# Optimization experiments

Hardware: AMD Instinct MI355X
Metric: run time of the kernel (lower is better)

## Reference

```python
import jax, jax.numpy as jnp
import numpy as np

EPS = 1e-5
NUM_GROUPS = 32


def setup_inputs() -> dict:
    key = jax.random.key(0)
    ks = jax.random.split(key, 4)
    b, c, h, w = 8, 512, 32, 32
    x = jax.random.normal(ks[0], (b, c, h, w), dtype=jnp.float32)
    gn_weight = jnp.ones((c,), dtype=jnp.float32)
    gn_bias = jnp.zeros((c,), dtype=jnp.float32)
    qkv_w = jax.random.normal(ks[1], (3 * c, c), dtype=jnp.float32) * (1.0 / np.sqrt(c))
    qkv_b = jnp.zeros((3 * c,), dtype=jnp.float32)
    proj_w = jax.random.normal(ks[2], (c, c), dtype=jnp.float32) * (1.0 / np.sqrt(c))
    proj_b = jnp.zeros((c,), dtype=jnp.float32)
    return {"x": x, "gn_weight": gn_weight, "gn_bias": gn_bias,
            "qkv_w": qkv_w, "qkv_b": qkv_b, "proj_w": proj_w, "proj_b": proj_b}


def _group_norm(x, weight, bias):
    b, c, h, w = x.shape
    xg = x.reshape(b, NUM_GROUPS, c // NUM_GROUPS, h, w)
    mean = xg.mean(axis=(2, 3, 4), keepdims=True)
    var = xg.var(axis=(2, 3, 4), keepdims=True)
    xn = ((xg - mean) * jax.lax.rsqrt(var + EPS)).reshape(b, c, h, w)
    return xn * weight[None, :, None, None] + bias[None, :, None, None]


def reference(x, gn_weight, gn_bias, qkv_w, qkv_b, proj_w, proj_b):
    b, c, h, w = x.shape
    scale = c ** (-0.5)
    xn = _group_norm(x, gn_weight, gn_bias)
    # 1x1 conv == per-pixel matmul over channels
    qkv = jnp.einsum('bchw,oc->bohw', xn, qkv_w) + qkv_b[None, :, None, None]
    q, k, v = jnp.split(qkv.reshape(b, 3 * c, h * w), 3, axis=1)  # each [b, c, N]
    attn = jax.nn.softmax(jnp.einsum('bci,bcj->bij', q, k) * scale, axis=-1)
    out = jnp.einsum('bij,bcj->bci', attn, v).reshape(b, c, h, w)
    proj = jnp.einsum('bchw,oc->bohw', out, proj_w) + proj_b[None, :, None, None]
    return x + proj
```

## Files before the change

### kernel.cpp

```cpp
#include <hip/hip_runtime.h>
#include <cmath>

constexpr int Bsz = 8, Cch = 512, NPIX = 1024;
constexpr int NG = 32, CPG = 16;

typedef __attribute__((ext_vector_type(4))) float f32x4;
typedef __attribute__((ext_vector_type(8))) short s16x8;

#define GLOBAL_AS __attribute__((address_space(1)))
#define LDS_AS __attribute__((address_space(3)))

__device__ inline short f2bf(float f) {
  union { float f; unsigned u; } c = {f};
  unsigned r = (c.u + 0x7fffu + ((c.u >> 16) & 1u)) >> 16;
  return (short)r;
}

__device__ inline float wave_reduce_sum(float v) {
#pragma unroll
  for (int off = 32; off > 0; off >>= 1) v += __shfl_xor(v, off, 64);
  return v;
}
__device__ inline float wave_reduce_max(float v) {
#pragma unroll
  for (int off = 32; off > 0; off >>= 1) v = fmaxf(v, __shfl_xor(v, off, 64));
  return v;
}

__global__ __launch_bounds__(256) void cvt_kernel(const float* __restrict__ in1,
                                                  short* __restrict__ out1, int n1,
                                                  const float* __restrict__ in2,
                                                  short* __restrict__ out2, int n2) {
  const int i = (blockIdx.x * 256 + threadIdx.x) * 4;
  const float* in = in1;
  short* out = out1;
  int j = i;
  if (i >= n1) { in = in2; out = out2; j = i - n1; }
  if (j + 3 < (i >= n1 ? n2 : n1)) {
    float4 v = *(const float4*)(in + j);
    short o[4] = {f2bf(v.x), f2bf(v.y), f2bf(v.z), f2bf(v.w)};
    *(uint2*)(out + j) = *(const uint2*)o;
  }
}

__global__ __launch_bounds__(256) void gn_kernel(
    const float* __restrict__ x, const float* __restrict__ w,
    const float* __restrict__ bb, short* __restrict__ xnt) {
  __shared__ float sm[8];
  const int bg = blockIdx.x, b = bg >> 5, g = bg & 31;
  const float* xp = x + ((size_t)(b * Cch + g * CPG)) * NPIX;
  float s = 0.f, ss = 0.f;
  for (int i = threadIdx.x * 4; i < CPG * NPIX; i += 1024) {
    float4 v = *(const float4*)(xp + i);
    s += v.x + v.y + v.z + v.w;
    ss += v.x * v.x + v.y * v.y + v.z * v.z + v.w * v.w;
  }
  s = wave_reduce_sum(s);
  ss = wave_reduce_sum(ss);
  const int wv = threadIdx.x >> 6;
  if ((threadIdx.x & 63) == 0) { sm[wv] = s; sm[4 + wv] = ss; }
  __syncthreads();
  const float tsum = sm[0] + sm[1] + sm[2] + sm[3];
  const float tsq = sm[4] + sm[5] + sm[6] + sm[7];
  const float inv_n = 1.0f / (CPG * NPIX);
  const float mean = tsum * inv_n;
  const float rstd = rsqrtf(tsq * inv_n - mean * mean + 1e-5f);
  float wc[CPG], bc[CPG];
#pragma unroll
  for (int c = 0; c < CPG; ++c) {
    wc[c] = w[g * CPG + c] * rstd;
    bc[c] = bb[g * CPG + c] - mean * wc[c];
  }
  for (int p = threadIdx.x; p < NPIX; p += 256) {
    short ov[CPG];
#pragma unroll
    for (int c = 0; c < CPG; ++c)
      ov[c] = f2bf(xp[(size_t)c * NPIX + p] * wc[c] + bc[c]);
    short* op = xnt + ((size_t)(b * NPIX + p)) * Cch + g * CPG;
    *(uint4*)op = *(const uint4*)&ov[0];
    *(uint4*)(op + 8) = *(const uint4*)&ov[8];
  }
}

template <int BM, int BN, int EPI>
__global__ __launch_bounds__(256) void mfma_gemm(
    const short* __restrict__ A, const short* __restrict__ B, int K, int lda,
    int ldb, long sA, long sB, const float* __restrict__ bias, float alpha,
    void* __restrict__ Cp, long sC, int ldc, void* __restrict__ C2p, long sC2,
    const float* __restrict__ resid, long sR) {
  constexpr int FM = BM / 32, FN = BN / 32;
  constexpr int NA = BM / 64, NB = BN / 64;
  __shared__ __align__(16) short Asl[BM * 32];
  __shared__ __align__(16) short Bsl[BN * 32];
  const int t = threadIdx.x;
  const int lane = t & 63, wave = t >> 6;
  const int bz = blockIdx.z;
  const int m0 = blockIdx.y * BM, n0 = blockIdx.x * BN;
  A += sA * bz;
  B += sB * bz;

  const short* ga[NA];
  const short* gb[NB];
  short* la[NA];
  short* lb[NB];
#pragma unroll
  for (int i = 0; i < NA; ++i) {
    const int s = i * 256 + t;
    const int row = ((s >> 6) * 16) + (s & 15);
    const int q = (s >> 4) & 3;
    ga[i] = A + (size_t)(m0 + row) * lda + q * 8;
    la[i] = Asl + s * 8;
  }
#pragma unroll
  for (int i = 0; i < NB; ++i) {
    const int s = i * 256 + t;
    const int row = ((s >> 6) * 16) + (s & 15);
    const int q = (s >> 4) & 3;
    gb[i] = B + (size_t)(n0 + row) * ldb + q * 8;
    lb[i] = Bsl + s * 8;
  }

  f32x4 acc[FM][FN] = {};
  const int wm = wave & 1, wn = wave >> 1;

  for (int k0 = 0; k0 < K; k0 += 32) {
#pragma unroll
    for (int i = 0; i < NA; ++i) {
      __builtin_amdgcn_global_load_lds((const GLOBAL_AS void*)ga[i],
                                       (LDS_AS void*)la[i], 16, 0, 0);
      ga[i] += 32;
    }
#pragma unroll
    for (int i = 0; i < NB; ++i) {
      __builtin_amdgcn_global_load_lds((const GLOBAL_AS void*)gb[i],
                                       (LDS_AS void*)lb[i], 16, 0, 0);
      gb[i] += 32;
    }
    __syncthreads();
    s16x8 af[FM], bf[FN];
#pragma unroll
    for (int i = 0; i < FM; ++i)
      af[i] = *(const s16x8*)(Asl + (wm * FM + i) * 512 + lane * 8);
#pragma unroll
    for (int i = 0; i < FN; ++i)
      bf[i] = *(const s16x8*)(Bsl + (wn * FN + i) * 512 + lane * 8);
#pragma unroll
    for (int im = 0; im < FM; ++im)
#pragma unroll
      for (int in = 0; in < FN; ++in)
        acc[im][in] = __builtin_amdgcn_mfma_f32_16x16x32_bf16(
            af[im], bf[in], acc[im][in], 0, 0, 0);
    __syncthreads();
  }

  const int quad = lane >> 4, nn = lane & 15;
#pragma unroll
  for (int im = 0; im < FM; ++im) {
#pragma unroll
    for (int in = 0; in < FN; ++in) {
      const int m = m0 + (wm * FM + im) * 16 + quad * 4;
      const int n = n0 + (wn * FN + in) * 16 + nn;
      if (EPI == 0) {
        if (m0 < 1024) {
          short* Cq = (short*)Cp + sC * bz;
          short o[4];
#pragma unroll
          for (int r = 0; r < 4; ++r) o[r] = f2bf(acc[im][in][r] + bias[m + r]);
          *(uint2*)(Cq + (size_t)n * ldc + m) = *(const uint2*)o;
        } else {
          short* Cv = (short*)C2p + sC2 * bz;
#pragma unroll
          for (int r = 0; r < 4; ++r)
            Cv[(size_t)(m - 1024 + r) * ldc + n] =
                f2bf(acc[im][in][r] + bias[m + r]);
        }
      } else if (EPI == 1) {
        float* Cf = (float*)Cp + sC * bz;
#pragma unroll
        for (int r = 0; r < 4; ++r)
          Cf[(size_t)(m + r) * ldc + n] = acc[im][in][r] * alpha;
      } else if (EPI == 2) {
        short* Cs = (short*)Cp + sC * bz;
#pragma unroll
        for (int r = 0; r < 4; ++r)
          Cs[(size_t)(m + r) * ldc + n] = f2bf(acc[im][in][r]);
      } else {
        float* Cf = (float*)Cp + sC * bz;
        const float* R = resid + sR * bz;
#pragma unroll
        for (int r = 0; r < 4; ++r)
          Cf[(size_t)(m + r) * ldc + n] =
              acc[im][in][r] + bias[m + r] + R[(size_t)(m + r) * ldc + n];
      }
    }
  }
}

__global__ __launch_bounds__(256) void softmax_kernel(const float* __restrict__ S,
                                                      short* __restrict__ P) {
  __shared__ float sm[8];
  const float* p = S + (size_t)blockIdx.x * 1024;
  const int t = threadIdx.x;
  float4 v = ((const float4*)p)[t];
  float mx = fmaxf(fmaxf(v.x, v.y), fmaxf(v.z, v.w));
  mx = wave_reduce_max(mx);
  if ((t & 63) == 0) sm[t >> 6] = mx;
  __syncthreads();
  mx = fmaxf(fmaxf(sm[0], sm[1]), fmaxf(sm[2], sm[3]));
  v.x = __expf(v.x - mx);
  v.y = __expf(v.y - mx);
  v.z = __expf(v.z - mx);
  v.w = __expf(v.w - mx);
  float s = v.x + v.y + v.z + v.w;
  s = wave_reduce_sum(s);
  if ((t & 63) == 0) sm[4 + (t >> 6)] = s;
  __syncthreads();
  const float inv = 1.0f / (sm[4] + sm[5] + sm[6] + sm[7]);
  short o[4] = {f2bf(v.x * inv), f2bf(v.y * inv), f2bf(v.z * inv),
                f2bf(v.w * inv)};
  *(uint2*)(P + (size_t)blockIdx.x * 1024 + t * 4) = *(const uint2*)o;
}

extern "C" void kernel_launch(void* const* d_in, const int* in_sizes, int n_in,
                              void* d_out, int out_size, void* d_ws,
                              size_t ws_size, hipStream_t stream) {
  const float* x = (const float*)d_in[0];
  const float* gnw = (const float*)d_in[1];
  const float* gnb = (const float*)d_in[2];
  const float* qkvw = (const float*)d_in[3];
  const float* qkvb = (const float*)d_in[4];
  const float* projw = (const float*)d_in[5];
  const float* projb = (const float*)d_in[6];
  float* out = (float*)d_out;

  char* ws = (char*)d_ws;
  short* xnt = (short*)ws;
  short* qkt = (short*)(ws + (8ull << 20));
  short* vbuf = (short*)(ws + (24ull << 20));
  float* Sbuf = (float*)(ws + (32ull << 20));
  short* Pbuf = (short*)(ws + (64ull << 20));
  short* Ot = (short*)(ws + (80ull << 20));
  short* wq = (short*)(ws + (88ull << 20));
  short* wp = (short*)(ws + (89ull << 20) + (512ull << 10));

  cvt_kernel<<<1024, 256, 0, stream>>>(qkvw, wq, 1536 * 512, projw, wp,
                                       512 * 512);

  gn_kernel<<<Bsz * NG, 256, 0, stream>>>(x, gnw, gnb, xnt);

  mfma_gemm<128, 128, 0><<<dim3(8, 12, Bsz), 256, 0, stream>>>(
      wq, xnt, 512, 512, 512, 0L, 1024L * 512, qkvb, 1.0f, qkt, 1024L * 1024,
      1024, vbuf, 512L * 1024, nullptr, 0L);

  const float scale = 1.0f / sqrtf(512.0f);
  mfma_gemm<128, 128, 1><<<dim3(8, 8, Bsz), 256, 0, stream>>>(
      qkt, qkt + 512, 512, 1024, 1024, 1024L * 1024, 1024L * 1024, nullptr,
      scale, Sbuf, 1024L * 1024, 1024, nullptr, 0L, nullptr, 0L);

  softmax_kernel<<<Bsz * 1024, 256, 0, stream>>>(Sbuf, Pbuf);

  mfma_gemm<128, 64, 2><<<dim3(8, 8, Bsz), 256, 0, stream>>>(
      Pbuf, vbuf, 1024, 1024, 1024, 1024L * 1024, 512L * 1024, nullptr, 1.0f,
      Ot, 1024L * 512, 512, nullptr, 0L, nullptr, 0L);

  mfma_gemm<64, 128, 3><<<dim3(8, 8, Bsz), 256, 0, stream>>>(
      wp, Ot, 512, 512, 512, 0L, 1024L * 512, projb, 1.0f, out, 512L * 1024,
      1024, nullptr, 0L, x, 512L * 1024);
}
```

Before: 202.3 us.

## Double-buffer LDS tiles in MFMA GEMM to overlap loads with compute

Splits the shared-memory A and B tiles into two buffers. The next K-slice is prefetched with global_load_lds while MFMAs run on the current slice. This cuts the per-iteration barriers from two to one and is meant to hide global-load latency behind matrix math. In exchange it doubles LDS use per block, which can lower occupancy. The overlap may also be lost if the compiler inserts a full vmcnt wait before the LDS reads.

```diff
diff --git a/kernel.cpp b/kernel.cpp
--- a/kernel.cpp
+++ b/kernel.cpp
@@ -90,8 +90,8 @@
     const float* __restrict__ resid, long sR) {
   constexpr int FM = BM / 32, FN = BN / 32;
   constexpr int NA = BM / 64, NB = BN / 64;
-  __shared__ __align__(16) short Asl[BM * 32];
-  __shared__ __align__(16) short Bsl[BN * 32];
+  __shared__ __align__(16) short Asl[2][BM * 32];
+  __shared__ __align__(16) short Bsl[2][BN * 32];
   const int t = threadIdx.x;
   const int lane = t & 63, wave = t >> 6;
   const int bz = blockIdx.z;
@@ -101,56 +101,62 @@
 
   const short* ga[NA];
   const short* gb[NB];
-  short* la[NA];
-  short* lb[NB];
+  int lofA[NA], lofB[NB];
 #pragma unroll
   for (int i = 0; i < NA; ++i) {
     const int s = i * 256 + t;
-    const int row = ((s >> 6) * 16) + (s & 15);
-    const int q = (s >> 4) & 3;
-    ga[i] = A + (size_t)(m0 + row) * lda + q * 8;
-    la[i] = Asl + s * 8;
+    ga[i] = A + (size_t)(m0 + ((s >> 6) * 16) + (s & 15)) * lda + ((s >> 4) & 3) * 8;
+    lofA[i] = s * 8;
   }
 #pragma unroll
   for (int i = 0; i < NB; ++i) {
     const int s = i * 256 + t;
-    const int row = ((s >> 6) * 16) + (s & 15);
-    const int q = (s >> 4) & 3;
-    gb[i] = B + (size_t)(n0 + row) * ldb + q * 8;
-    lb[i] = Bsl + s * 8;
-  }
+    gb[i] = B + (size_t)(n0 + ((s >> 6) * 16) + (s & 15)) * ldb + ((s >> 4) & 3) * 8;
+    lofB[i] = s * 8;
+  }
+
+#pragma unroll
+  for (int i = 0; i < NA; ++i)
+    __builtin_amdgcn_global_load_lds((const GLOBAL_AS void*)ga[i],
+                                     (LDS_AS void*)&Asl[0][lofA[i]], 16, 0, 0);
+#pragma unroll
+  for (int i = 0; i < NB; ++i)
+    __builtin_amdgcn_global_load_lds((const GLOBAL_AS void*)gb[i],
+                                     (LDS_AS void*)&Bsl[0][lofB[i]], 16, 0, 0);
 
   f32x4 acc[FM][FN] = {};
   const int wm = wave & 1, wn = wave >> 1;
+  int cur = 0;
 
   for (int k0 = 0; k0 < K; k0 += 32) {
-#pragma unroll
-    for (int i = 0; i < NA; ++i) {
-      __builtin_amdgcn_global_load_lds((const GLOBAL_AS void*)ga[i],
-                                       (LDS_AS void*)la[i], 16, 0, 0);
-      ga[i] += 32;
+    __syncthreads();
+    if (k0 + 32 < K) {
+      const int nxt = cur ^ 1;
+#pragma unroll
+      for (int i = 0; i < NA; ++i)
+        __builtin_amdgcn_global_load_lds(
+            (const GLOBAL_AS void*)(ga[i] + k0 + 32),
+            (LDS_AS void*)&Asl[nxt][lofA[i]], 16, 0, 0);
+#pragma unroll
+      for (int i = 0; i < NB; ++i)
+        __builtin_amdgcn_global_load_lds(
+            (const GLOBAL_AS void*)(gb[i] + k0 + 32),
+            (LDS_AS void*)&Bsl[nxt][lofB[i]], 16, 0, 0);
     }
-#pragma unroll
-    for (int i = 0; i < NB; ++i) {
-      __builtin_amdgcn_global_load_lds((const GLOBAL_AS void*)gb[i],
-                                       (LDS_AS void*)lb[i], 16, 0, 0);
-      gb[i] += 32;
-    }
-    __syncthreads();
     s16x8 af[FM], bf[FN];
 #pragma unroll
     for (int i = 0; i < FM; ++i)
-      af[i] = *(const s16x8*)(Asl + (wm * FM + i) * 512 + lane * 8);
+      af[i] = *(const s16x8*)(&Asl[cur][(wm * FM + i) * 512 + lane * 8]);
 #pragma unroll
     for (int i = 0; i < FN; ++i)
-      bf[i] = *(const s16x8*)(Bsl + (wn * FN + i) * 512 + lane * 8);
+      bf[i] = *(const s16x8*)(&Bsl[cur][(wn * FN + i) * 512 + lane * 8]);
 #pragma unroll
     for (int im = 0; im < FM; ++im)
 #pragma unroll
       for (int in = 0; in < FN; ++in)
         acc[im][in] = __builtin_amdgcn_mfma_f32_16x16x32_bf16(
             af[im], bf[in], acc[im][in], 0, 0, 0);
-    __syncthreads();
+    cur ^= 1;
   }
 
   const int quad = lane >> 4, nn = lane & 15;
```

New measurement: 206.5 us. 1.02x slower.
